# Performance work log

Measured on AMD Instinct MI355X. Metric: run time of the kernel, lower is better.

Reference implementation:

```python
import jax, jax.numpy as jnp
import numpy as np

NEG_SLOPE = 0.2
BN_EPS = 1e-5


def gat_conv(x, src, dst, W, att_src, att_dst, bias):
    """PyG-style GATConv (eval mode, shared src/dst lin, self-loops already in src/dst)."""
    N = x.shape[0]
    H, C = att_src.shape
    h = (x @ W).reshape(N, H, C)                      # [N,H,C]
    a_s = jnp.sum(h * att_src[None], axis=-1)         # [N,H]
    a_d = jnp.sum(h * att_dst[None], axis=-1)         # [N,H]
    e = jax.nn.leaky_relu(a_s[src] + a_d[dst], NEG_SLOPE)   # [E,H]
    # segment softmax over edges grouped by destination node
    m = jax.ops.segment_max(e, dst, num_segments=N)   # [N,H]
    ee = jnp.exp(e - m[dst])
    denom = jax.ops.segment_sum(ee, dst, num_segments=N)
    alpha = ee / (denom[dst] + 1e-16)                 # [E,H]
    msg = h[src] * alpha[..., None]                   # [E,H,C]
    out = jax.ops.segment_sum(msg, dst, num_segments=N)  # [N,H,C]
    return out.reshape(N, H * C) + bias


def setup_inputs() -> dict:
    key = jax.random.key(0)
    ks = jax.random.split(key, 12)
    N, E, Fin, C1, H, Fout = 50000, 800000, 128, 16, 8, 40
    HC = H * C1
    x = jax.random.normal(ks[0], (N, Fin), jnp.float32)
    edge_index = jax.random.randint(ks[1], (2, E), 0, N, dtype=jnp.int32)
    W1 = jax.random.normal(ks[2], (Fin, HC), jnp.float32) / np.sqrt(Fin).astype(np.float32)
    att_src1 = jax.random.normal(ks[3], (H, C1), jnp.float32) * 0.1
    att_dst1 = jax.random.normal(ks[4], (H, C1), jnp.float32) * 0.1
    b1 = jnp.zeros((HC,), jnp.float32)
    bn_gamma = jnp.ones((HC,), jnp.float32)
    bn_beta = jnp.zeros((HC,), jnp.float32)
    bn_mean = jnp.zeros((HC,), jnp.float32)
    bn_var = jnp.ones((HC,), jnp.float32)
    W2 = jax.random.normal(ks[5], (HC, Fout), jnp.float32) / np.sqrt(HC).astype(np.float32)
    att_src2 = jax.random.normal(ks[6], (1, Fout), jnp.float32) * 0.1
    att_dst2 = jax.random.normal(ks[7], (1, Fout), jnp.float32) * 0.1
    b2 = jnp.zeros((Fout,), jnp.float32)
    return {"x": x, "edge_index": edge_index, "W1": W1, "att_src1": att_src1,
            "att_dst1": att_dst1, "b1": b1, "bn_gamma": bn_gamma, "bn_beta": bn_beta,
            "bn_mean": bn_mean, "bn_var": bn_var, "W2": W2, "att_src2": att_src2,
            "att_dst2": att_dst2, "b2": b2}


def reference(x, edge_index, W1, att_src1, att_dst1, b1, bn_gamma, bn_beta,
              bn_mean, bn_var, W2, att_src2, att_dst2, b2):
    N = x.shape[0]
    loop = jnp.arange(N, dtype=edge_index.dtype)
    src = jnp.concatenate([edge_index[0], loop])   # PyG add_self_loops=True
    dst = jnp.concatenate([edge_index[1], loop])
    h = gat_conv(x, src, dst, W1, att_src1, att_dst1, b1)
    h = (h - bn_mean) * jax.lax.rsqrt(bn_var + BN_EPS) * bn_gamma + bn_beta  # BN eval
    h = jax.nn.elu(h)
    out = gat_conv(h, src, dst, W2, att_src2, att_dst2, b2)
    return jax.nn.log_softmax(out, axis=1)
```

## Files before the change

### kernel.cpp

```cpp
#include <hip/hip_runtime.h>
#include <hip/hip_bf16.h>
#include <math.h>

#define LRELU(v) ((v) > 0.f ? (v) : 0.2f * (v))

typedef __attribute__((ext_vector_type(8))) short bf16x8;
typedef __attribute__((ext_vector_type(4))) float f32x4;

__device__ inline unsigned int f2bf(float f) {
  unsigned int u = __float_as_uint(f);
  return (u + 0x7fffu + ((u >> 16) & 1u)) >> 16;
}

__global__ __launch_bounds__(256) void wtrans_k(const float* __restrict__ W,
                                                unsigned short* __restrict__ wt)
{
  int idx = blockIdx.x * 256 + threadIdx.x;
  int k = idx >> 7, c = idx & 127;
  wt[c * 128 + k] = (unsigned short)f2bf(W[idx]);
}

#define LDA 152
__global__ __launch_bounds__(256) void gemm1_k(
    const float* __restrict__ x, const unsigned short* __restrict__ wt,
    const float* __restrict__ atts, const float* __restrict__ attd,
    unsigned short* __restrict__ h1s, float* __restrict__ as1,
    float* __restrict__ ad1, int N)
{
  __shared__ unsigned short xs[64 * LDA];
  const int t = threadIdx.x;
  const int row0 = blockIdx.x * 64;
  const int lane = t & 63, w = t >> 6;

#pragma unroll
  for (int i = 0; i < 8; ++i) {
    int idx = t + i * 256;
    int r = idx >> 5, kq = idx & 31;
    int rr = row0 + r;
    float4 v = make_float4(0.f, 0.f, 0.f, 0.f);
    if (rr < N) v = *reinterpret_cast<const float4*>(&x[(size_t)rr * 128 + kq * 4]);
    unsigned int p0 = f2bf(v.x) | (f2bf(v.y) << 16);
    unsigned int p1 = f2bf(v.z) | (f2bf(v.w) << 16);
    *reinterpret_cast<uint2*>(&xs[r * LDA + kq * 4]) = make_uint2(p0, p1);
  }
  __syncthreads();

  const int l16 = lane & 15, lhi = lane >> 4;
  const int nb0 = w * 32;
  f32x4 acc[4][2];
#pragma unroll
  for (int m = 0; m < 4; ++m)
#pragma unroll
    for (int n = 0; n < 2; ++n) acc[m][n] = (f32x4){0.f, 0.f, 0.f, 0.f};

#pragma unroll
  for (int ks = 0; ks < 4; ++ks) {
    bf16x8 bf[2];
#pragma unroll
    for (int n = 0; n < 2; ++n) {
      int col = nb0 + n * 16 + l16;
      bf[n] = *reinterpret_cast<const bf16x8*>(&wt[col * 128 + ks * 32 + 8 * lhi]);
    }
#pragma unroll
    for (int m = 0; m < 4; ++m) {
      bf16x8 af = *reinterpret_cast<const bf16x8*>(
          &xs[(m * 16 + l16) * LDA + ks * 32 + 8 * lhi]);
      acc[m][0] = __builtin_amdgcn_mfma_f32_16x16x32_bf16(af, bf[0], acc[m][0], 0, 0, 0);
      acc[m][1] = __builtin_amdgcn_mfma_f32_16x16x32_bf16(af, bf[1], acc[m][1], 0, 0, 0);
    }
  }

#pragma unroll
  for (int n = 0; n < 2; ++n) {
    int col = nb0 + n * 16 + l16;
    float av = atts[col], dv = attd[col];
    int head = w * 2 + n;
#pragma unroll
    for (int m = 0; m < 4; ++m) {
#pragma unroll
      for (int r = 0; r < 4; ++r) {
        int row = row0 + m * 16 + lhi * 4 + r;
        float v = acc[m][n][r];
        float s = v * av, d = v * dv;
        s += __shfl_xor(s, 1); s += __shfl_xor(s, 2);
        s += __shfl_xor(s, 4); s += __shfl_xor(s, 8);
        d += __shfl_xor(d, 1); d += __shfl_xor(d, 2);
        d += __shfl_xor(d, 4); d += __shfl_xor(d, 8);
        if (row < N) {
          h1s[(size_t)row * 128 + col] = (unsigned short)f2bf(v);
          if (l16 == 0) { as1[row * 8 + head] = s; ad1[row * 8 + head] = d; }
        }
      }
    }
  }
}

#define NBUK_MAX 256

__global__ __launch_bounds__(256) void bhist_k(const int* __restrict__ ei,
                                               int E, int N,
                                               int* __restrict__ bcnt, int nbuk)
{
  __shared__ int h[NBUK_MAX];
  for (int i = threadIdx.x; i < nbuk; i += 256) h[i] = 0;
  __syncthreads();
  const int Etot = E + N;
  const int base = blockIdx.x * 4096;
#pragma unroll 4
  for (int i = threadIdx.x; i < 4096; i += 256) {
    int e = base + i;
    if (e < Etot) {
      int d = (e < E) ? ei[E + e] : (e - E);
      atomicAdd(&h[d >> 8], 1);
    }
  }
  __syncthreads();
  for (int i = threadIdx.x; i < nbuk; i += 256)
    if (h[i]) atomicAdd(&bcnt[i], h[i]);
}

__global__ __launch_bounds__(256) void bscan_k(const int* __restrict__ bcnt,
                                               int* __restrict__ bbase,
                                               int* __restrict__ bpos, int nbuk)
{
  __shared__ int wsum[4], wtot[4];
  const int t = threadIdx.x, lane = t & 63, w = t >> 6;
  int v = (t < nbuk) ? bcnt[t] : 0;
  int incl = v;
#pragma unroll
  for (int off = 1; off < 64; off <<= 1) {
    int y = __shfl_up(incl, off);
    if (lane >= off) incl += y;
  }
  if (lane == 63) wtot[w] = incl;
  __syncthreads();
  if (t == 0) {
    int a = wtot[0], b = wtot[1], c = wtot[2];
    wsum[0] = 0; wsum[1] = a; wsum[2] = a + b; wsum[3] = a + b + c;
  }
  __syncthreads();
  int ex = wsum[w] + incl - v;
  if (t < nbuk) { bbase[t] = ex; bpos[t] = ex; }
  if (t == nbuk - 1) bbase[nbuk] = ex + v;
}

__global__ __launch_bounds__(256) void bscat_k(const int* __restrict__ ei,
                                               int E, int N,
                                               int* __restrict__ bpos,
                                               unsigned int* __restrict__ stg,
                                               int nbuk)
{
  __shared__ int h[NBUK_MAX], gp[NBUK_MAX], cur[NBUK_MAX];
  for (int i = threadIdx.x; i < nbuk; i += 256) { h[i] = 0; cur[i] = 0; }
  __syncthreads();
  const int Etot = E + N;
  const int base = blockIdx.x * 4096;
  int s[16], d[16];
#pragma unroll
  for (int i = 0; i < 16; ++i) {
    int e = base + i * 256 + threadIdx.x;
    if (e < Etot) {
      if (e < E) { s[i] = ei[e]; d[i] = ei[E + e]; }
      else       { s[i] = d[i] = e - E; }
      atomicAdd(&h[d[i] >> 8], 1);
    } else d[i] = -1;
  }
  __syncthreads();
  for (int i = threadIdx.x; i < nbuk; i += 256)
    gp[i] = h[i] ? atomicAdd(&bpos[i], h[i]) : 0;
  __syncthreads();
#pragma unroll
  for (int i = 0; i < 16; ++i) {
    if (d[i] >= 0) {
      int b = d[i] >> 8;
      int r = atomicAdd(&cur[b], 1);
      stg[gp[b] + r] = ((unsigned int)s[i] << 8) | (unsigned int)(d[i] & 255);
    }
  }
}

#define CCAP 4992
__global__ __launch_bounds__(512) void csr_k(const unsigned int* __restrict__ stg,
                                             const int* __restrict__ bbase,
                                             int* __restrict__ rowptr,
                                             int* __restrict__ col,
                                             int N, int nbuk)
{
  __shared__ int nh[256], nb[257], cur[256], wsum[4];
  __shared__ int cstage[CCAP];
  const int b = blockIdx.x, t = threadIdx.x;
  const int n0 = b << 8;
  const int e0 = bbase[b], e1 = bbase[b + 1], cnt = e1 - e0;
  if (t < 256) { nh[t] = 0; cur[t] = 0; }
  __syncthreads();
  for (int i = t; i < cnt; i += 512)
    atomicAdd(&nh[stg[e0 + i] & 255u], 1);
  __syncthreads();
  if (t < 256) {
    const int lane = t & 63, w = t >> 6;
    int v = nh[t], incl = v;
#pragma unroll
    for (int off = 1; off < 64; off <<= 1) {
      int y = __shfl_up(incl, off);
      if (lane >= off) incl += y;
    }
    if (lane == 63) wsum[w] = incl;
    __syncthreads();
    if (t == 0) {
      int a = wsum[0], bb = wsum[1], c = wsum[2];
      wsum[0] = 0; wsum[1] = a; wsum[2] = a + bb; wsum[3] = a + bb + c;
    }
    __syncthreads();
    int ex = wsum[w] + incl - v;
    nb[t] = ex;
    if (t == 255) nb[256] = ex + v;
  } else {
    __syncthreads();
    __syncthreads();
  }
  __syncthreads();
  const int nnodes = min(256, N - n0);
  for (int i = t; i < nnodes; i += 512) rowptr[n0 + i] = e0 + nb[i];
  if (b == nbuk - 1 && t == 0) rowptr[N] = e1;
  for (int i = t; i < cnt; i += 512) {
    unsigned int sd = stg[e0 + i];
    int li = sd & 255u;
    int p = nb[li] + atomicAdd(&cur[li], 1);
    int sv = (int)(sd >> 8);
    if (p < CCAP) cstage[p] = sv; else col[e0 + p] = sv;
  }
  __syncthreads();
  const int lim = min(cnt, CCAP);
  for (int i = t; i < lim; i += 512) col[e0 + i] = cstage[i];
}

__global__ __launch_bounds__(256) void agg1_k(
    const unsigned int* __restrict__ h1b, const float* __restrict__ as1,
    const float* __restrict__ ad1, const int* __restrict__ rowptr,
    const int* __restrict__ col, const float* __restrict__ b1,
    const float* __restrict__ gamma, const float* __restrict__ beta,
    const float* __restrict__ mean, const float* __restrict__ var,
    float* __restrict__ hmid, int N)
{
  const int wid = threadIdx.x >> 6, lane = threadIdx.x & 63;
  const int n = blockIdx.x * 4 + wid;
  if (n >= N) return;
  const int h = lane >> 3;
  const int c0 = lane * 2;
  const float adv = ad1[n * 8 + h];
  float den = 0.f, a0 = 0.f, a1 = 0.f;
  const int jb = rowptr[n], je = rowptr[n + 1];
  int j = jb;
  for (; j + 8 <= je; j += 8) {
    int s[8];
#pragma unroll
    for (int q = 0; q < 8; ++q) s[q] = col[j + q];
    float e[8];
#pragma unroll
    for (int q = 0; q < 8; ++q) e[q] = as1[s[q] * 8 + h];
    unsigned int u[8];
#pragma unroll
    for (int q = 0; q < 8; ++q) u[q] = h1b[s[q] * 64 + lane];
#pragma unroll
    for (int q = 0; q < 8; ++q) {
      float p = __expf(LRELU(e[q] + adv));
      den += p;
      a0 += p * __uint_as_float(u[q] << 16);
      a1 += p * __uint_as_float(u[q] & 0xffff0000u);
    }
  }
  for (; j < je; ++j) {
    int s = col[j];
    float e = LRELU(as1[s * 8 + h] + adv);
    unsigned int u = h1b[s * 64 + lane];
    float p = __expf(e);
    den += p;
    a0 += p * __uint_as_float(u << 16);
    a1 += p * __uint_as_float(u & 0xffff0000u);
  }
  float r = 1.f / (den + 1e-16f);
  float o0 = a0 * r + b1[c0];
  float o1 = a1 * r + b1[c0 + 1];
  float bn0 = (o0 - mean[c0]) * rsqrtf(var[c0] + 1e-5f) * gamma[c0] + beta[c0];
  float bn1 = (o1 - mean[c0 + 1]) * rsqrtf(var[c0 + 1] + 1e-5f) * gamma[c0 + 1] + beta[c0 + 1];
  float2 o;
  o.x = bn0 > 0.f ? bn0 : expm1f(bn0);
  o.y = bn1 > 0.f ? bn1 : expm1f(bn1);
  *reinterpret_cast<float2*>(&hmid[n * 128 + c0]) = o;
}

__global__ __launch_bounds__(256) void gemm2_k(
    const float* __restrict__ hmid, const float* __restrict__ W2,
    const float* __restrict__ atts, const float* __restrict__ attd,
    float* __restrict__ h2p, float* __restrict__ as2, float* __restrict__ ad2,
    int N)
{
  __shared__ float hm[128 * 36];
  __shared__ float w2t[40 * 36];
  const int t = threadIdx.x;
  const int n0 = blockIdx.x * 128;
  const int lane = t & 63, w = t >> 6;
  const int ng = lane >> 3, cg = lane & 7;
  const int nloc = w * 32 + ng * 4;

  float acc[4][5];
#pragma unroll
  for (int i = 0; i < 4; ++i)
#pragma unroll
    for (int j = 0; j < 5; ++j) acc[i][j] = 0.f;

  for (int kc = 0; kc < 4; ++kc) {
    __syncthreads();
#pragma unroll
    for (int i = 0; i < 4; ++i) {
      int idx = t + i * 256;
      int r = idx >> 3, kq = idx & 7;
      int rr = n0 + r;
      float4 v = make_float4(0.f, 0.f, 0.f, 0.f);
      if (rr < N)
        v = *reinterpret_cast<const float4*>(&hmid[(size_t)rr * 128 + kc * 32 + kq * 4]);
      *reinterpret_cast<float4*>(&hm[r * 36 + kq * 4]) = v;
    }
#pragma unroll
    for (int i = 0; i < 5; ++i) {
      int flat = t + i * 256;
      int c = flat >> 5, kk = flat & 31;
      w2t[c * 36 + kk] = W2[(size_t)(kc * 32 + kk) * 40 + c];
    }
    __syncthreads();
#pragma unroll
    for (int k4 = 0; k4 < 8; ++k4) {
      float hv[4][4];
#pragma unroll
      for (int i = 0; i < 4; ++i)
        *reinterpret_cast<float4*>(hv[i]) =
            *reinterpret_cast<const float4*>(&hm[(nloc + i) * 36 + k4 * 4]);
      float wv[5][4];
#pragma unroll
      for (int j = 0; j < 5; ++j)
        *reinterpret_cast<float4*>(wv[j]) =
            *reinterpret_cast<const float4*>(&w2t[(cg * 5 + j) * 36 + k4 * 4]);
#pragma unroll
      for (int i = 0; i < 4; ++i)
#pragma unroll
        for (int j = 0; j < 5; ++j)
#pragma unroll
          for (int kk = 0; kk < 4; ++kk)
            acc[i][j] += hv[i][kk] * wv[j][kk];
    }
  }

  float asv[5], adv[5];
#pragma unroll
  for (int j = 0; j < 5; ++j) { asv[j] = atts[cg * 5 + j]; adv[j] = attd[cg * 5 + j]; }
#pragma unroll
  for (int i = 0; i < 4; ++i) {
    int n = n0 + nloc + i;
    if (n >= N) continue;
    float ps = 0.f, pd = 0.f;
#pragma unroll
    for (int j = 0; j < 5; ++j) { ps += acc[i][j] * asv[j]; pd += acc[i][j] * adv[j]; }
#pragma unroll
    for (int off = 1; off < 8; off <<= 1) {
      ps += __shfl_xor(ps, off);
      pd += __shfl_xor(pd, off);
    }
#pragma unroll
    for (int j = 0; j < 5; ++j) h2p[(size_t)n * 40 + cg * 5 + j] = acc[i][j];
    if (cg == 0) { as2[n] = ps; ad2[n] = pd; }
  }
}

__global__ __launch_bounds__(256) void agg2_k(
    const float* __restrict__ h2p, const float* __restrict__ as2,
    const float* __restrict__ ad2, const int* __restrict__ rowptr,
    const int* __restrict__ col, const float* __restrict__ b2,
    float* __restrict__ out, int N)
{
  const int wid = threadIdx.x >> 6, lane = threadIdx.x & 63;
  const int n = blockIdx.x * 4 + wid;
  if (n >= N) return;
  const bool act = lane < 40;
  const int cl = act ? lane : 39;
  const float adv = ad2[n];
  float den = 0.f, acc = 0.f;
  const int jb = rowptr[n], je = rowptr[n + 1];
  int j = jb;
  for (; j + 4 <= je; j += 4) {
    int s0 = col[j], s1 = col[j + 1], s2 = col[j + 2], s3 = col[j + 3];
    float e0 = as2[s0], e1 = as2[s1], e2 = as2[s2], e3 = as2[s3];
    float v0 = h2p[s0 * 40 + cl];
    float v1 = h2p[s1 * 40 + cl];
    float v2 = h2p[s2 * 40 + cl];
    float v3 = h2p[s3 * 40 + cl];
    e0 = LRELU(e0 + adv); e1 = LRELU(e1 + adv);
    e2 = LRELU(e2 + adv); e3 = LRELU(e3 + adv);
    float p0 = __expf(e0), p1 = __expf(e1);
    float p2 = __expf(e2), p3 = __expf(e3);
    den += p0; den += p1; den += p2; den += p3;
    acc += p0 * v0; acc += p1 * v1; acc += p2 * v2; acc += p3 * v3;
  }
  for (; j < je; ++j) {
    int s = col[j];
    float e = LRELU(as2[s] + adv);
    float v = h2p[s * 40 + cl];
    float p = __expf(e);
    den += p;
    acc += p * v;
  }
  float o = acc / (den + 1e-16f) + b2[cl];
  float mv = act ? o : -INFINITY;
#pragma unroll
  for (int off = 1; off < 64; off <<= 1) mv = fmaxf(mv, __shfl_xor(mv, off));
  float ex = act ? __expf(o - mv) : 0.f;
#pragma unroll
  for (int off = 1; off < 64; off <<= 1) ex += __shfl_xor(ex, off);
  float ls = logf(ex);
  if (act) out[n * 40 + lane] = o - mv - ls;
}

extern "C" void kernel_launch(void* const* d_in, const int* in_sizes, int n_in,
                              void* d_out, int out_size, void* d_ws,
                              size_t ws_size, hipStream_t stream)
{
  const float* x      = (const float*)d_in[0];
  const int*   ei     = (const int*)d_in[1];
  const float* W1     = (const float*)d_in[2];
  const float* att_s1 = (const float*)d_in[3];
  const float* att_d1 = (const float*)d_in[4];
  const float* b1     = (const float*)d_in[5];
  const float* gamma  = (const float*)d_in[6];
  const float* beta   = (const float*)d_in[7];
  const float* mean   = (const float*)d_in[8];
  const float* var    = (const float*)d_in[9];
  const float* W2     = (const float*)d_in[10];
  const float* att_s2 = (const float*)d_in[11];
  const float* att_d2 = (const float*)d_in[12];
  const float* b2     = (const float*)d_in[13];
  float* out = (float*)d_out;

  const int N = in_sizes[0] / 128;
  const int E = in_sizes[1] / 2;
  const int Etot = E + N;
  const int nbuk = (N + 255) >> 8;
  const int nchunk = (Etot + 4095) / 4096;

  char* ws = (char*)d_ws;
  size_t off = 0;
  auto alloc = [&](size_t bytes) -> void* {
    void* p = ws + off;
    off = (off + bytes + 255) & ~(size_t)255;
    return p;
  };
  unsigned short* h1s = (unsigned short*)alloc((size_t)N * 128 * 2);
  float* as1  = (float*)alloc((size_t)N * 8 * 4);
  float* ad1  = (float*)alloc((size_t)N * 8 * 4);
  float* hmid = (float*)alloc((size_t)N * 128 * 4);
  int* rowptr = (int*)alloc((size_t)(N + 1) * 4);
  int* col    = (int*)alloc((size_t)Etot * 4);
  unsigned int* stg = (unsigned int*)alloc((size_t)Etot * 4);
  int* bcnt   = (int*)alloc(NBUK_MAX * 4);
  int* bbase  = (int*)alloc((NBUK_MAX + 1) * 4);
  int* bpos   = (int*)alloc(NBUK_MAX * 4);
  unsigned short* wt = (unsigned short*)alloc(16384 * 2);
  float* h2p = (float*)h1s;
  float* as2 = as1;
  float* ad2 = ad1;

  hipMemsetAsync(bcnt, 0, NBUK_MAX * 4, stream);

  wtrans_k<<<64, 256, 0, stream>>>(W1, wt);
  gemm1_k<<<(N + 63) / 64, 256, 0, stream>>>(x, wt, att_s1, att_d1,
                                             h1s, as1, ad1, N);
  bhist_k<<<nchunk, 256, 0, stream>>>(ei, E, N, bcnt, nbuk);
  bscan_k<<<1, 256, 0, stream>>>(bcnt, bbase, bpos, nbuk);
  bscat_k<<<nchunk, 256, 0, stream>>>(ei, E, N, bpos, stg, nbuk);
  csr_k<<<nbuk, 512, 0, stream>>>(stg, bbase, rowptr, col, N, nbuk);

  agg1_k<<<(N + 3) / 4, 256, 0, stream>>>((const unsigned int*)h1s, as1, ad1,
                                          rowptr, col, b1,
                                          gamma, beta, mean, var, hmid, N);
  gemm2_k<<<(N + 127) / 128, 256, 0, stream>>>(hmid, W2, att_s2, att_d2,
                                               h2p, as2, ad2, N);
  agg2_k<<<(N + 3) / 4, 256, 0, stream>>>(h2p, as2, ad2, rowptr, col, b2,
                                          out, N);
}
```

Baseline: 178.6 us.

## Split each wavefront into two half-waves processing alternate edges with wider loads

Both aggregation kernels now split the 64-lane wavefront into two halves. Each half handles alternating neighbor edges and loads wider vectors per lane (uint2 of bf16 in layer 1, float2 in layer 2), and the halves are combined with a cross-half shuffle at the end. The goal is more independent gathers in flight per node and better lane utilization in the 40-wide layer 2, where previously 24 lanes sat idle. The cost is predicated tail handling, extra shuffle reductions, and half the lanes staying idle during the epilogue.

```diff
diff --git a/kernel.cpp b/kernel.cpp
--- a/kernel.cpp
+++ b/kernel.cpp
@@ -11,6 +11,8 @@
   unsigned int u = __float_as_uint(f);
   return (u + 0x7fffu + ((u >> 16) & 1u)) >> 16;
 }
+__device__ inline float bf_lo(unsigned int u) { return __uint_as_float(u << 16); }
+__device__ inline float bf_hi(unsigned int u) { return __uint_as_float(u & 0xffff0000u); }
 
 __global__ __launch_bounds__(256) void wtrans_k(const float* __restrict__ W,
                                                 unsigned short* __restrict__ wt)
@@ -245,48 +247,63 @@
   const int wid = threadIdx.x >> 6, lane = threadIdx.x & 63;
   const int n = blockIdx.x * 4 + wid;
   if (n >= N) return;
-  const int h = lane >> 3;
-  const int c0 = lane * 2;
+  const int eh = lane >> 5;
+  const int cl = lane & 31;
+  const int h  = cl >> 2;
   const float adv = ad1[n * 8 + h];
-  float den = 0.f, a0 = 0.f, a1 = 0.f;
+  float den = 0.f, a0 = 0.f, a1 = 0.f, a2 = 0.f, a3 = 0.f;
   const int jb = rowptr[n], je = rowptr[n + 1];
-  int j = jb;
-  for (; j + 8 <= je; j += 8) {
-    int s[8];
-#pragma unroll
-    for (int q = 0; q < 8; ++q) s[q] = col[j + q];
-    float e[8];
-#pragma unroll
-    for (int q = 0; q < 8; ++q) e[q] = as1[s[q] * 8 + h];
-    unsigned int u[8];
-#pragma unroll
-    for (int q = 0; q < 8; ++q) u[q] = h1b[s[q] * 64 + lane];
-#pragma unroll
-    for (int q = 0; q < 8; ++q) {
-      float p = __expf(LRELU(e[q] + adv));
+  for (int j = jb; j < je; j += 8) {
+    int s[4]; bool v[4];
+#pragma unroll
+    for (int q = 0; q < 4; ++q) {
+      int idx = j + 2 * q + eh;
+      v[q] = idx < je;
+      s[q] = col[v[q] ? idx : je - 1];
+    }
+    float e[4];
+#pragma unroll
+    for (int q = 0; q < 4; ++q) e[q] = as1[s[q] * 8 + h];
+    uint2 u[4];
+#pragma unroll
+    for (int q = 0; q < 4; ++q)
+      u[q] = *reinterpret_cast<const uint2*>(&h1b[s[q] * 64 + cl * 2]);
+#pragma unroll
+    for (int q = 0; q < 4; ++q) {
+      float p = v[q] ? __expf(LRELU(e[q] + adv)) : 0.f;
       den += p;
-      a0 += p * __uint_as_float(u[q] << 16);
-      a1 += p * __uint_as_float(u[q] & 0xffff0000u);
-    }
-  }
-  for (; j < je; ++j) {
-    int s = col[j];
-    float e = LRELU(as1[s * 8 + h] + adv);
-    unsigned int u = h1b[s * 64 + lane];
-    float p = __expf(e);
-    den += p;
-    a0 += p * __uint_as_float(u << 16);
-    a1 += p * __uint_as_float(u & 0xffff0000u);
-  }
-  float r = 1.f / (den + 1e-16f);
-  float o0 = a0 * r + b1[c0];
-  float o1 = a1 * r + b1[c0 + 1];
-  float bn0 = (o0 - mean[c0]) * rsqrtf(var[c0] + 1e-5f) * gamma[c0] + beta[c0];
-  float bn1 = (o1 - mean[c0 + 1]) * rsqrtf(var[c0 + 1] + 1e-5f) * gamma[c0 + 1] + beta[c0 + 1];
-  float2 o;
-  o.x = bn0 > 0.f ? bn0 : expm1f(bn0);
-  o.y = bn1 > 0.f ? bn1 : expm1f(bn1);
-  *reinterpret_cast<float2*>(&hmid[n * 128 + c0]) = o;
+      a0 += p * bf_lo(u[q].x);
+      a1 += p * bf_hi(u[q].x);
+      a2 += p * bf_lo(u[q].y);
+      a3 += p * bf_hi(u[q].y);
+    }
+  }
+  den += __shfl_xor(den, 32);
+  a0 += __shfl_xor(a0, 32);
+  a1 += __shfl_xor(a1, 32);
+  a2 += __shfl_xor(a2, 32);
+  a3 += __shfl_xor(a3, 32);
+  if (eh == 0) {
+    const int c0 = cl * 4;
+    float r = 1.f / (den + 1e-16f);
+    float4 bb = *reinterpret_cast<const float4*>(&b1[c0]);
+    float4 mm = *reinterpret_cast<const float4*>(&mean[c0]);
+    float4 vv = *reinterpret_cast<const float4*>(&var[c0]);
+    float4 gg = *reinterpret_cast<const float4*>(&gamma[c0]);
+    float4 be = *reinterpret_cast<const float4*>(&beta[c0]);
+    float o0 = a0 * r + bb.x, o1 = a1 * r + bb.y;
+    float o2 = a2 * r + bb.z, o3 = a3 * r + bb.w;
+    float n0 = (o0 - mm.x) * rsqrtf(vv.x + 1e-5f) * gg.x + be.x;
+    float n1 = (o1 - mm.y) * rsqrtf(vv.y + 1e-5f) * gg.y + be.y;
+    float n2 = (o2 - mm.z) * rsqrtf(vv.z + 1e-5f) * gg.z + be.z;
+    float n3 = (o3 - mm.w) * rsqrtf(vv.w + 1e-5f) * gg.w + be.w;
+    float4 o;
+    o.x = n0 > 0.f ? n0 : expm1f(n0);
+    o.y = n1 > 0.f ? n1 : expm1f(n1);
+    o.z = n2 > 0.f ? n2 : expm1f(n2);
+    o.w = n3 > 0.f ? n3 : expm1f(n3);
+    *reinterpret_cast<float4*>(&hmid[n * 128 + c0]) = o;
+  }
 }
 
 __global__ __launch_bounds__(256) void gemm2_k(
@@ -380,43 +397,54 @@
   const int wid = threadIdx.x >> 6, lane = threadIdx.x & 63;
   const int n = blockIdx.x * 4 + wid;
   if (n >= N) return;
-  const bool act = lane < 40;
-  const int cl = act ? lane : 39;
+  const int eh = lane >> 5;
+  const int cl = lane & 31;
+  const bool actc = cl < 20;
+  const int c0 = (actc ? cl : 19) * 2;
   const float adv = ad2[n];
-  float den = 0.f, acc = 0.f;
+  float den = 0.f, a0 = 0.f, a1 = 0.f;
   const int jb = rowptr[n], je = rowptr[n + 1];
-  int j = jb;
-  for (; j + 4 <= je; j += 4) {
-    int s0 = col[j], s1 = col[j + 1], s2 = col[j + 2], s3 = col[j + 3];
-    float e0 = as2[s0], e1 = as2[s1], e2 = as2[s2], e3 = as2[s3];
-    float v0 = h2p[s0 * 40 + cl];
-    float v1 = h2p[s1 * 40 + cl];
-    float v2 = h2p[s2 * 40 + cl];
-    float v3 = h2p[s3 * 40 + cl];
-    e0 = LRELU(e0 + adv); e1 = LRELU(e1 + adv);
-    e2 = LRELU(e2 + adv); e3 = LRELU(e3 + adv);
-    float p0 = __expf(e0), p1 = __expf(e1);
-    float p2 = __expf(e2), p3 = __expf(e3);
-    den += p0; den += p1; den += p2; den += p3;
-    acc += p0 * v0; acc += p1 * v1; acc += p2 * v2; acc += p3 * v3;
-  }
-  for (; j < je; ++j) {
-    int s = col[j];
-    float e = LRELU(as2[s] + adv);
-    float v = h2p[s * 40 + cl];
-    float p = __expf(e);
-    den += p;
-    acc += p * v;
-  }
-  float o = acc / (den + 1e-16f) + b2[cl];
-  float mv = act ? o : -INFINITY;
-#pragma unroll
-  for (int off = 1; off < 64; off <<= 1) mv = fmaxf(mv, __shfl_xor(mv, off));
-  float ex = act ? __expf(o - mv) : 0.f;
-#pragma unroll
-  for (int off = 1; off < 64; off <<= 1) ex += __shfl_xor(ex, off);
+  for (int j = jb; j < je; j += 8) {
+    int s[4]; bool v[4];
+#pragma unroll
+    for (int q = 0; q < 4; ++q) {
+      int idx = j + 2 * q + eh;
+      v[q] = idx < je;
+      s[q] = col[v[q] ? idx : je - 1];
+    }
+    float e[4];
+#pragma unroll
+    for (int q = 0; q < 4; ++q) e[q] = as2[s[q]];
+    float2 f[4];
+#pragma unroll
+    for (int q = 0; q < 4; ++q)
+      f[q] = *reinterpret_cast<const float2*>(&h2p[s[q] * 40 + c0]);
+#pragma unroll
+    for (int q = 0; q < 4; ++q) {
+      float p = v[q] ? __expf(LRELU(e[q] + adv)) : 0.f;
+      den += p;
+      a0 += p * f[q].x;
+      a1 += p * f[q].y;
+    }
+  }
+  den += __shfl_xor(den, 32);
+  a0 += __shfl_xor(a0, 32);
+  a1 += __shfl_xor(a1, 32);
+  float r = 1.f / (den + 1e-16f);
+  float o0 = a0 * r + b2[c0];
+  float o1 = a1 * r + b2[c0 + 1];
+  const bool act = actc && (eh == 0);
+  float mv = act ? fmaxf(o0, o1) : -INFINITY;
+#pragma unroll
+  for (int off = 1; off < 32; off <<= 1) mv = fmaxf(mv, __shfl_xor(mv, off));
+  float ex = act ? (__expf(o0 - mv) + __expf(o1 - mv)) : 0.f;
+#pragma unroll
+  for (int off = 1; off < 32; off <<= 1) ex += __shfl_xor(ex, off);
   float ls = logf(ex);
-  if (act) out[n * 40 + lane] = o - mv - ls;
+  if (act) {
+    float2 ov = make_float2(o0 - mv - ls, o1 - mv - ls);
+    *reinterpret_cast<float2*>(&out[n * 40 + c0]) = ov;
+  }
 }
 
 extern "C" void kernel_launch(void* const* d_in, const int* in_sizes, int n_in,
```

After: 167.4 us. 1.07x faster.
